# Optimization experiments

Hardware: AMD Instinct MI355X
Metric: run time of the kernel (lower is better)

## Reference

```python
import jax, jax.numpy as jnp
import numpy as np

N = 10000       # nodes
E = 640000      # edges (avg degree 64)
F_IN = 128      # num_node_features
H = 128         # hid_size
C = 16          # num_classes


def setup_inputs() -> dict:
    key = jax.random.key(0)
    ks = jax.random.split(key, 12)
    g = lambda k, shape, fan: jax.random.normal(k, shape, jnp.float32) * (1.0 / np.sqrt(fan))
    return {
        "x": jax.random.normal(ks[0], (N, F_IN), jnp.float32),
        "edge_index": jax.random.randint(ks[1], (2, E), 0, N, dtype=jnp.int32),
        "W1": g(ks[2], (F_IN, H), F_IN), "b1": jnp.zeros((H,), jnp.float32),
        "W2": g(ks[3], (H, H), H),       "b2": jnp.zeros((H,), jnp.float32),
        "Wlin1": g(ks[4], (H, C), H),    "blin1": jnp.zeros((C,), jnp.float32),
        "Wdeg2": g(ks[5], (H, 1), H),    "bdeg2": jnp.zeros((1,), jnp.float32),
        "Wdeg3": g(ks[6], (H, 1), H),    "bdeg3": jnp.zeros((1,), jnp.float32),
        "Wdown": g(ks[7], (F_IN, H), F_IN), "bdown": jnp.zeros((H,), jnp.float32),
    }


def _gcn_norm(edge_index):
    # PyG GCNConv: add self-loops, symmetric normalization d^-1/2 A d^-1/2
    loops = jnp.arange(N, dtype=edge_index.dtype)
    src = jnp.concatenate([edge_index[0], loops])   # [E+N]
    dst = jnp.concatenate([edge_index[1], loops])   # [E+N]
    deg = jax.ops.segment_sum(jnp.ones_like(dst, jnp.float32), dst, num_segments=N)
    dis = jnp.where(deg > 0, jax.lax.rsqrt(jnp.maximum(deg, 1.0)), 0.0)
    norm = dis[src] * dis[dst]                      # [E+N]
    return src, dst, norm


def _gcn_conv(h, W, b, src, dst, norm):
    h = h @ W                                       # [N, H] transform first (smaller dim)
    msg = h[src] * norm[:, None]                    # gather + edge weight
    return jax.ops.segment_sum(msg, dst, num_segments=N) + b


def reference(x, edge_index, W1, b1, W2, b2, Wlin1, blin1, Wdeg2, bdeg2, Wdeg3, bdeg3, Wdown, bdown):
    src, dst, norm = _gcn_norm(edge_index)
    original = x @ Wdown + bdown                    # down_sample residual
    h = jax.nn.relu(_gcn_conv(x, W1, b1, src, dst, norm))
    # dropout is identity in eval mode
    h = _gcn_conv(h, W2, b2, src, dst, norm) + original
    result1 = jax.nn.log_softmax(h @ Wlin1 + blin1, axis=1)   # [N, C]
    result2 = (h @ Wdeg2 + bdeg2)[:, 0]                        # [N]
    result3 = (h @ Wdeg3 + bdeg3)[:, 0]                        # [N]
    return (result1, result2, result3)
```

## Files before the change

kernel.cpp:

```cpp
#include <hip/hip_runtime.h>
#include <math.h>

#define N_NODES 10000
#define N_EDGES 640000
#define NB      100
#define CH      (N_EDGES / NB)
#define HP      10016
#define GB      313
#define NBLK    40
#define NPB2    250

typedef unsigned short ushort4_t __attribute__((ext_vector_type(4)));
typedef unsigned short ushort8_t __attribute__((ext_vector_type(8)));

__device__ inline unsigned short f2bf(float f) {
    unsigned int u = __float_as_uint(f);
    u = (u + 0x7FFFu + ((u >> 16) & 1u)) >> 16;
    return (unsigned short)u;
}
__device__ inline float bf2f(unsigned short s) {
    return __uint_as_float(((unsigned int)s) << 16);
}

__device__ __forceinline__ void gbar(int* bar, int slot, int nblk) {
    __syncthreads();
    if (threadIdx.x == 0) {
        int* cnt = bar + slot;
        int* gen = bar + 8 + slot;
        int g = atomicAdd(gen, 0);
        __threadfence();
        if (atomicAdd(cnt, 1) == nblk - 1) {
            __threadfence();
            atomicAdd(gen, 1);
        } else {
            while (atomicAdd(gen, 0) == g) __builtin_amdgcn_s_sleep(4);
        }
        __threadfence();
    }
    __syncthreads();
}

__global__ __launch_bounds__(256) void k_hist_gemm2(const int* __restrict__ dst,
                                                    unsigned short* __restrict__ hmat,
                                                    unsigned short* __restrict__ rank,
                                                    int* __restrict__ bar,
                                                    const float* __restrict__ X,
                                                    const float* __restrict__ W1,
                                                    const float* __restrict__ Wdown,
                                                    const float* __restrict__ bdown,
                                                    unsigned short* __restrict__ outT,
                                                    float* __restrict__ outB, int n) {
    __shared__ char smem[81920];
    int t = threadIdx.x;

    if (blockIdx.x < NB) {
        int* hs = (int*)smem;
        if (blockIdx.x == 0 && t < 16) bar[t] = 0;
        for (int j = t; j < HP; j += 256) hs[j] = 0;
        __syncthreads();
        int base = blockIdx.x * CH;
#pragma unroll 4
        for (int j = t; j < CH; j += 256) {
            int r = atomicAdd(&hs[dst[base + j]], 1);
            rank[base + j] = (unsigned short)r;
        }
        __syncthreads();
        unsigned short* out = hmat + blockIdx.x * HP;
        for (int j = t; j < N_NODES; j += 256) out[j] = (unsigned short)hs[j];
        return;
    }

    float* xs = (float*)smem;
    float* wsm = (float*)(smem + 16384);
    int bid = blockIdx.x - NB;
    int which = (bid >= GB) ? 1 : 0;
    int bx = which ? bid - GB : bid;
    int tile0 = bx * 32;
    const float* W = which ? Wdown : W1;

    const float4* Wv = (const float4*)W;
    float4* wsv = (float4*)wsm;
#pragma unroll
    for (int q = 0; q < 16; ++q) wsv[t + 256 * q] = Wv[t + 256 * q];

    const float4* Xv = (const float4*)X;
    float4* xsv = (float4*)xs;
#pragma unroll
    for (int q = 0; q < 4; ++q) {
        int idx = t + 256 * q;
        int row = tile0 + (idx >> 5);
        float4 v = make_float4(0.f, 0.f, 0.f, 0.f);
        if (row < n) v = Xv[(size_t)row * 32 + (idx & 31)];
        xsv[idx] = v;
    }
    __syncthreads();

    int c4 = t & 31;
    int rg = t >> 5;
    float4 acc[4];
#pragma unroll
    for (int p = 0; p < 4; ++p) acc[p] = make_float4(0.f, 0.f, 0.f, 0.f);

    const float4* wsr = (const float4*)wsm;
    const float4* xsr = (const float4*)xs;
#pragma unroll 4
    for (int kq = 0; kq < 32; ++kq) {
        float4 w0 = wsr[(4 * kq + 0) * 32 + c4];
        float4 w1 = wsr[(4 * kq + 1) * 32 + c4];
        float4 w2 = wsr[(4 * kq + 2) * 32 + c4];
        float4 w3 = wsr[(4 * kq + 3) * 32 + c4];
#pragma unroll
        for (int p = 0; p < 4; ++p) {
            float4 xv = xsr[(rg * 4 + p) * 32 + kq];
            acc[p].x += xv.x * w0.x + xv.y * w1.x + xv.z * w2.x + xv.w * w3.x;
            acc[p].y += xv.x * w0.y + xv.y * w1.y + xv.z * w2.y + xv.w * w3.y;
            acc[p].z += xv.x * w0.z + xv.y * w1.z + xv.z * w2.z + xv.w * w3.z;
            acc[p].w += xv.x * w0.w + xv.y * w1.w + xv.z * w2.w + xv.w * w3.w;
        }
    }
    if (which == 0) {
#pragma unroll
        for (int p = 0; p < 4; ++p) {
            int row = tile0 + rg * 4 + p;
            if (row < n) {
                ushort4_t o;
                o[0] = f2bf(acc[p].x); o[1] = f2bf(acc[p].y);
                o[2] = f2bf(acc[p].z); o[3] = f2bf(acc[p].w);
                ((ushort4_t*)outT)[(size_t)row * 32 + c4] = o;
            }
        }
    } else {
        float4 bv = ((const float4*)bdown)[c4];
#pragma unroll
        for (int p = 0; p < 4; ++p) {
            int row = tile0 + rg * 4 + p;
            if (row < n) {
                float4 o;
                o.x = acc[p].x + bv.x; o.y = acc[p].y + bv.y;
                o.z = acc[p].z + bv.z; o.w = acc[p].w + bv.w;
                ((float4*)outB)[(size_t)row * 32 + c4] = o;
            }
        }
    }
}

__global__ __launch_bounds__(256) void k_mid(const unsigned short* __restrict__ h,
                                             int* bar,
                                             int* __restrict__ rangesum,
                                             int* __restrict__ offsets,
                                             float* __restrict__ dis,
                                             int* __restrict__ bmat) {
    __shared__ int sc[256];
    __shared__ int rsl[NBLK];
    __shared__ int sP;
    int b = blockIdx.x, t = threadIdx.x;
    int i = b * NPB2 + t;
    bool act = (t < NPB2);

    int s = 0;
    if (act) {
#pragma unroll 10
        for (int bb = 0; bb < NB; ++bb) s += h[bb * HP + i];
        dis[i] = rsqrtf((float)(s + 1));
    }
    sc[t] = s;
    __syncthreads();
#pragma unroll
    for (int off = 1; off < 256; off <<= 1) {
        int v = (t >= off) ? sc[t - off] : 0;
        __syncthreads();
        sc[t] += v;
        __syncthreads();
    }
    int lofs = sc[t] - s;
    if (t == 255) rangesum[b] = sc[255];
    gbar(bar, 0, NBLK);

    if (t < NBLK) rsl[t] = rangesum[t];
    __syncthreads();
    if (t == 0) {
        int P = 0;
        for (int bb = 0; bb < b; ++bb) P += rsl[bb];
        sP = P;
        if (b == NBLK - 1) offsets[N_NODES] = P + rsl[b];
    }
    __syncthreads();
    if (act) {
        int run = sP + lofs;
        offsets[i] = run;
#pragma unroll 10
        for (int bb = 0; bb < NB; ++bb) {
            bmat[bb * HP + i] = run;
            run += h[bb * HP + i];
        }
    }
}

__global__ __launch_bounds__(256) void k_scatter_ep(const int* __restrict__ src,
                                                    const int* __restrict__ dst,
                                                    const unsigned short* __restrict__ rank,
                                                    const int* __restrict__ bmat,
                                                    const float* __restrict__ dis,
                                                    int2* __restrict__ rec) {
    int e = blockIdx.x * 256 + threadIdx.x;
    int b = blockIdx.x / (CH / 256);
    int d = dst[e];
    int s = src[e];
    int r = rank[e];
    int pos = bmat[b * HP + d] + r;
    rec[pos] = make_int2(s, __float_as_int(dis[s]));
}

__global__ __launch_bounds__(256) void k_gemm(const float* __restrict__ X,
                                              const float* __restrict__ W,
                                              unsigned short* __restrict__ Y, int n) {
    __shared__ float xs[32 * 128];
    __shared__ float ws[128 * 128];
    int t = threadIdx.x;
    int tile0 = blockIdx.x * 32;

    const float4* Wv = (const float4*)W;
    float4* wsv = (float4*)ws;
#pragma unroll
    for (int q = 0; q < 16; ++q) wsv[t + 256 * q] = Wv[t + 256 * q];

    const float4* Xv = (const float4*)X;
    float4* xsv = (float4*)xs;
#pragma unroll
    for (int q = 0; q < 4; ++q) {
        int idx = t + 256 * q;
        int row = tile0 + (idx >> 5);
        float4 v = make_float4(0.f, 0.f, 0.f, 0.f);
        if (row < n) v = Xv[(size_t)row * 32 + (idx & 31)];
        xsv[idx] = v;
    }
    __syncthreads();

    int c4 = t & 31;
    int rg = t >> 5;
    float4 acc[4];
#pragma unroll
    for (int p = 0; p < 4; ++p) acc[p] = make_float4(0.f, 0.f, 0.f, 0.f);

    const float4* wsr = (const float4*)ws;
    const float4* xsr = (const float4*)xs;
#pragma unroll 4
    for (int kq = 0; kq < 32; ++kq) {
        float4 w0 = wsr[(4 * kq + 0) * 32 + c4];
        float4 w1 = wsr[(4 * kq + 1) * 32 + c4];
        float4 w2 = wsr[(4 * kq + 2) * 32 + c4];
        float4 w3 = wsr[(4 * kq + 3) * 32 + c4];
#pragma unroll
        for (int p = 0; p < 4; ++p) {
            float4 xv = xsr[(rg * 4 + p) * 32 + kq];
            acc[p].x += xv.x * w0.x + xv.y * w1.x + xv.z * w2.x + xv.w * w3.x;
            acc[p].y += xv.x * w0.y + xv.y * w1.y + xv.z * w2.y + xv.w * w3.y;
            acc[p].z += xv.x * w0.z + xv.y * w1.z + xv.z * w2.z + xv.w * w3.z;
            acc[p].w += xv.x * w0.w + xv.y * w1.w + xv.z * w2.w + xv.w * w3.w;
        }
    }
#pragma unroll
    for (int p = 0; p < 4; ++p) {
        int row = tile0 + rg * 4 + p;
        if (row < n) {
            ushort4_t o;
            o[0] = f2bf(acc[p].x); o[1] = f2bf(acc[p].y);
            o[2] = f2bf(acc[p].z); o[3] = f2bf(acc[p].w);
            ((ushort4_t*)Y)[(size_t)row * 32 + c4] = o;
        }
    }
}

#define AGG_EDGE_LOOP_B                                                        \
    float acc[8];                                                              \
    _Pragma("unroll") for (int j = 0; j < 8; ++j) acc[j] = 0.f;                \
    int e = e0 + es;                                                           \
    for (; e + 48 < e1; e += 64) {                                             \
        int2 r0 = rec[e], r1 = rec[e + 16], r2 = rec[e + 32], r3 = rec[e + 48];\
        float w0 = __int_as_float(r0.y), w1 = __int_as_float(r1.y);            \
        float w2 = __int_as_float(r2.y), w3 = __int_as_float(r3.y);            \
        ushort8_t v0 = T8[(size_t)r0.x * 16 + c8];                             \
        ushort8_t v1 = T8[(size_t)r1.x * 16 + c8];                             \
        ushort8_t v2 = T8[(size_t)r2.x * 16 + c8];                             \
        ushort8_t v3 = T8[(size_t)r3.x * 16 + c8];                             \
        _Pragma("unroll") for (int j = 0; j < 8; ++j)                          \
            acc[j] += w0 * bf2f(v0[j]) + w1 * bf2f(v1[j]) +                    \
                      w2 * bf2f(v2[j]) + w3 * bf2f(v3[j]);                     \
    }                                                                          \
    for (; e + 16 < e1; e += 32) {                                             \
        int2 r0 = rec[e], r1 = rec[e + 16];                                    \
        float w0 = __int_as_float(r0.y), w1 = __int_as_float(r1.y);            \
        ushort8_t v0 = T8[(size_t)r0.x * 16 + c8];                             \
        ushort8_t v1 = T8[(size_t)r1.x * 16 + c8];                             \
        _Pragma("unroll") for (int j = 0; j < 8; ++j)                          \
            acc[j] += w0 * bf2f(v0[j]) + w1 * bf2f(v1[j]);                     \
    }                                                                          \
    if (e < e1) {                                                              \
        int2 r0 = rec[e];                                                      \
        float w0 = __int_as_float(r0.y);                                       \
        ushort8_t v0 = T8[(size_t)r0.x * 16 + c8];                             \
        _Pragma("unroll") for (int j = 0; j < 8; ++j)                          \
            acc[j] += w0 * bf2f(v0[j]);                                        \
    }                                                                          \
    _Pragma("unroll") for (int j = 0; j < 8; ++j) {                            \
        acc[j] += __shfl_xor(acc[j], 16, 64);                                  \
        acc[j] += __shfl_xor(acc[j], 32, 64);                                  \
    }

__global__ __launch_bounds__(256) void k_agg1(const ushort8_t* __restrict__ T8,
                                              const float* __restrict__ dis,
                                              const int* __restrict__ offsets,
                                              const int2* __restrict__ rec,
                                              const float* __restrict__ bias,
                                              float* __restrict__ Y) {
    __shared__ float red[3][16][9];
    int i = blockIdx.x;
    int t = threadIdx.x;
    int c8 = t & 15;
    int es = t >> 4;
    int wave = t >> 6;
    int lane = t & 63;
    int e0 = offsets[i], e1 = offsets[i + 1];

    AGG_EDGE_LOOP_B

    if (wave > 0 && lane < 16) {
#pragma unroll
        for (int j = 0; j < 8; ++j) red[wave - 1][lane][j] = acc[j];
    }
    __syncthreads();
    if (wave == 0 && lane < 16) {
#pragma unroll
        for (int j = 0; j < 8; ++j)
            acc[j] += red[0][lane][j] + red[1][lane][j] + red[2][lane][j];

        float di = dis[i];
        ushort8_t sv = T8[(size_t)i * 16 + c8];
#pragma unroll
        for (int j = 0; j < 8; ++j) acc[j] += di * bf2f(sv[j]);
#pragma unroll
        for (int j = 0; j < 8; ++j)
            acc[j] = fmaxf(di * acc[j] + bias[c8 * 8 + j], 0.f);

        float4* Y4 = (float4*)Y;
        Y4[(size_t)i * 32 + c8 * 2]     = make_float4(acc[0], acc[1], acc[2], acc[3]);
        Y4[(size_t)i * 32 + c8 * 2 + 1] = make_float4(acc[4], acc[5], acc[6], acc[7]);
    }
}

__global__ __launch_bounds__(256) void k_agg2h(const ushort8_t* __restrict__ T8,
                                               const float* __restrict__ dis,
                                               const int* __restrict__ offsets,
                                               const int2* __restrict__ rec,
                                               const float* __restrict__ bias,
                                               const float* __restrict__ resid,
                                               const float* __restrict__ Wlin,
                                               const float* __restrict__ blin,
                                               const float* __restrict__ Wd2,
                                               const float* __restrict__ bd2,
                                               const float* __restrict__ Wd3,
                                               const float* __restrict__ bd3,
                                               float* __restrict__ out1,
                                               float* __restrict__ out2,
                                               float* __restrict__ out3) {
    __shared__ float red[3][16][9];
    __shared__ float hrow[128];
    int i = blockIdx.x;
    int t = threadIdx.x;
    int c8 = t & 15;
    int es = t >> 4;
    int wave = t >> 6;
    int lane = t & 63;
    int e0 = offsets[i], e1 = offsets[i + 1];

    AGG_EDGE_LOOP_B

    if (wave > 0 && lane < 16) {
#pragma unroll
        for (int j = 0; j < 8; ++j) red[wave - 1][lane][j] = acc[j];
    }
    __syncthreads();
    if (wave == 0 && lane < 16) {
#pragma unroll
        for (int j = 0; j < 8; ++j)
            acc[j] += red[0][lane][j] + red[1][lane][j] + red[2][lane][j];

        float di = dis[i];
        ushort8_t sv = T8[(size_t)i * 16 + c8];
#pragma unroll
        for (int j = 0; j < 8; ++j) acc[j] += di * bf2f(sv[j]);

        const float4* rv4 = (const float4*)resid;
        float4 r0 = rv4[(size_t)i * 32 + c8 * 2];
        float4 r1 = rv4[(size_t)i * 32 + c8 * 2 + 1];
#pragma unroll
        for (int j = 0; j < 8; ++j) acc[j] = di * acc[j] + bias[c8 * 8 + j];
        acc[0] += r0.x; acc[1] += r0.y; acc[2] += r0.z; acc[3] += r0.w;
        acc[4] += r1.x; acc[5] += r1.y; acc[6] += r1.z; acc[7] += r1.w;

#pragma unroll
        for (int j = 0; j < 8; ++j) hrow[c8 * 8 + j] = acc[j];
    }
    __syncthreads();

    if (wave == 0) {
        float h0 = hrow[lane];
        float h1 = hrow[64 + lane];
        float p2 = h0 * Wd2[lane] + h1 * Wd2[64 + lane];
        float p3 = h0 * Wd3[lane] + h1 * Wd3[64 + lane];
#pragma unroll
        for (int d = 1; d < 64; d <<= 1) {
            p2 += __shfl_xor(p2, d, 64);
            p3 += __shfl_xor(p3, d, 64);
        }
        if (lane == 0) {
            out2[i] = p2 + bd2[0];
            out3[i] = p3 + bd3[0];
        }
        int c = lane & 15, kg = lane >> 4;
        float z = 0.f;
#pragma unroll 8
        for (int j = 0; j < 32; ++j) {
            int k = kg * 32 + j;
            z += hrow[k] * Wlin[k * 16 + c];
        }
        z += __shfl_xor(z, 16, 64);
        z += __shfl_xor(z, 32, 64);
        z += blin[c];
        float m = z;
#pragma unroll
        for (int d = 1; d < 16; d <<= 1) m = fmaxf(m, __shfl_xor(m, d, 64));
        float ex = expf(z - m);
        float ssum = ex;
#pragma unroll
        for (int d = 1; d < 16; d <<= 1) ssum += __shfl_xor(ssum, d, 64);
        float lsm = z - m - logf(ssum);
        if (lane < 16) out1[(size_t)i * 16 + c] = lsm;
    }
}

extern "C" void kernel_launch(void* const* d_in, const int* in_sizes, int n_in,
                              void* d_out, int out_size, void* d_ws, size_t ws_size,
                              hipStream_t stream) {
    const float* x     = (const float*)d_in[0];
    const int*   ei    = (const int*)d_in[1];
    const float* W1    = (const float*)d_in[2];
    const float* b1    = (const float*)d_in[3];
    const float* W2    = (const float*)d_in[4];
    const float* b2    = (const float*)d_in[5];
    const float* Wlin1 = (const float*)d_in[6];
    const float* blin1 = (const float*)d_in[7];
    const float* Wdeg2 = (const float*)d_in[8];
    const float* bdeg2 = (const float*)d_in[9];
    const float* Wdeg3 = (const float*)d_in[10];
    const float* bdeg3 = (const float*)d_in[11];
    const float* Wdown = (const float*)d_in[12];
    const float* bdown = (const float*)d_in[13];

    const int n = N_NODES, E = N_EDGES;
    const int* src = ei;
    const int* dst = ei + E;

    char* ws = (char*)d_ws;
    int*            bar      = (int*)ws;
    unsigned short* hmat     = (unsigned short*)(bar + 64);
    int*            bmat     = (int*)(hmat + NB * HP);
    int*            rangesum = bmat + NB * HP;
    int*            offsets  = rangesum + 64;
    float*          dis      = (float*)(offsets + 10048);
    unsigned short* rank     = (unsigned short*)(dis + HP);
    int2*           rec      = (int2*)(rank + E);
    unsigned short* bufT     = (unsigned short*)(rec + E);
    float*          bufB     = (float*)(bufT + (size_t)n * 128);
    float*          bufC     = bufB + (size_t)n * 128;

    k_hist_gemm2<<<NB + 2 * GB, 256, 0, stream>>>(dst, hmat, rank, bar, x, W1,
                                                  Wdown, bdown, bufT, bufB, n);
    k_mid<<<NBLK, 256, 0, stream>>>(hmat, bar, rangesum, offsets, dis, bmat);
    k_scatter_ep<<<E / 256, 256, 0, stream>>>(src, dst, rank, bmat, dis, rec);
    k_agg1<<<n, 256, 0, stream>>>((const ushort8_t*)bufT, dis, offsets, rec,
                                  b1, bufC);
    k_gemm<<<(n + 31) / 32, 256, 0, stream>>>(bufC, W2, bufT, n);
    float* out1 = (float*)d_out;
    float* out2 = out1 + (size_t)n * 16;
    float* out3 = out2 + n;
    k_agg2h<<<n, 256, 0, stream>>>((const ushort8_t*)bufT, dis, offsets, rec,
                                   b2, bufB, Wlin1, blin1, Wdeg2, bdeg2,
                                   Wdeg3, bdeg3, out1, out2, out3);
}
```

Baseline: 104.9 us.

## Fuse graph-build stages and agg1+GEMM into kernels joined by inter-block flags

```diff
diff --git a/kernel.cpp b/kernel.cpp
--- a/kernel.cpp
+++ b/kernel.cpp
@@ -9,6 +9,7 @@
 #define GB      313
 #define NBLK    40
 #define NPB2    250
+#define MID0    (NB + 2 * GB)
 
 typedef unsigned short ushort4_t __attribute__((ext_vector_type(4)));
 typedef unsigned short ushort8_t __attribute__((ext_vector_type(8)));
@@ -40,127 +41,139 @@
     __syncthreads();
 }
 
-__global__ __launch_bounds__(256) void k_hist_gemm2(const int* __restrict__ dst,
-                                                    unsigned short* __restrict__ hmat,
-                                                    unsigned short* __restrict__ rank,
-                                                    int* __restrict__ bar,
-                                                    const float* __restrict__ X,
-                                                    const float* __restrict__ W1,
-                                                    const float* __restrict__ Wdown,
-                                                    const float* __restrict__ bdown,
-                                                    unsigned short* __restrict__ outT,
-                                                    float* __restrict__ outB, int n) {
+__global__ __launch_bounds__(256) void k_front(const int* __restrict__ dst,
+                                               unsigned short* __restrict__ hmat,
+                                               unsigned short* __restrict__ rank,
+                                               int* bar,
+                                               const float* __restrict__ X,
+                                               const float* __restrict__ W1,
+                                               const float* __restrict__ Wdown,
+                                               const float* __restrict__ bdown,
+                                               unsigned short* __restrict__ outT,
+                                               float* __restrict__ outB,
+                                               int* __restrict__ rangesum,
+                                               int* __restrict__ offsets,
+                                               float* __restrict__ dis,
+                                               int* __restrict__ bmat, int n) {
     __shared__ char smem[81920];
     int t = threadIdx.x;
-
-    if (blockIdx.x < NB) {
+    int bid = blockIdx.x;
+
+    if (bid < NB) {
         int* hs = (int*)smem;
-        if (blockIdx.x == 0 && t < 16) bar[t] = 0;
+        if (bid == 0 && t < 16) bar[t] = 0;
         for (int j = t; j < HP; j += 256) hs[j] = 0;
         __syncthreads();
-        int base = blockIdx.x * CH;
+        int base = bid * CH;
 #pragma unroll 4
         for (int j = t; j < CH; j += 256) {
             int r = atomicAdd(&hs[dst[base + j]], 1);
             rank[base + j] = (unsigned short)r;
         }
         __syncthreads();
-        unsigned short* out = hmat + blockIdx.x * HP;
+        unsigned short* out = hmat + bid * HP;
         for (int j = t; j < N_NODES; j += 256) out[j] = (unsigned short)hs[j];
+        __syncthreads();
+        if (t == 0) {
+            __threadfence();
+            atomicExch(&bar[16 + bid], 1);
+        }
         return;
     }
 
-    float* xs = (float*)smem;
-    float* wsm = (float*)(smem + 16384);
-    int bid = blockIdx.x - NB;
-    int which = (bid >= GB) ? 1 : 0;
-    int bx = which ? bid - GB : bid;
-    int tile0 = bx * 32;
-    const float* W = which ? Wdown : W1;
-
-    const float4* Wv = (const float4*)W;
-    float4* wsv = (float4*)wsm;
-#pragma unroll
-    for (int q = 0; q < 16; ++q) wsv[t + 256 * q] = Wv[t + 256 * q];
-
-    const float4* Xv = (const float4*)X;
-    float4* xsv = (float4*)xs;
-#pragma unroll
-    for (int q = 0; q < 4; ++q) {
-        int idx = t + 256 * q;
-        int row = tile0 + (idx >> 5);
-        float4 v = make_float4(0.f, 0.f, 0.f, 0.f);
-        if (row < n) v = Xv[(size_t)row * 32 + (idx & 31)];
-        xsv[idx] = v;
-    }
-    __syncthreads();
-
-    int c4 = t & 31;
-    int rg = t >> 5;
-    float4 acc[4];
-#pragma unroll
-    for (int p = 0; p < 4; ++p) acc[p] = make_float4(0.f, 0.f, 0.f, 0.f);
-
-    const float4* wsr = (const float4*)wsm;
-    const float4* xsr = (const float4*)xs;
+    if (bid < MID0) {
+        float* xs = (float*)smem;
+        float* wsm = (float*)(smem + 16384);
+        int gid = bid - NB;
+        int which = (gid >= GB) ? 1 : 0;
+        int bx = which ? gid - GB : gid;
+        int tile0 = bx * 32;
+        const float* W = which ? Wdown : W1;
+
+        const float4* Wv = (const float4*)W;
+        float4* wsv = (float4*)wsm;
+#pragma unroll
+        for (int q = 0; q < 16; ++q) wsv[t + 256 * q] = Wv[t + 256 * q];
+
+        const float4* Xv = (const float4*)X;
+        float4* xsv = (float4*)xs;
+#pragma unroll
+        for (int q = 0; q < 4; ++q) {
+            int idx = t + 256 * q;
+            int row = tile0 + (idx >> 5);
+            float4 v = make_float4(0.f, 0.f, 0.f, 0.f);
+            if (row < n) v = Xv[(size_t)row * 32 + (idx & 31)];
+            xsv[idx] = v;
+        }
+        __syncthreads();
+
+        int c4 = t & 31;
+        int rg = t >> 5;
+        float4 acc[4];
+#pragma unroll
+        for (int p = 0; p < 4; ++p) acc[p] = make_float4(0.f, 0.f, 0.f, 0.f);
+
+        const float4* wsr = (const float4*)wsm;
+        const float4* xsr = (const float4*)xs;
 #pragma unroll 4
-    for (int kq = 0; kq < 32; ++kq) {
-        float4 w0 = wsr[(4 * kq + 0) * 32 + c4];
-        float4 w1 = wsr[(4 * kq + 1) * 32 + c4];
-        float4 w2 = wsr[(4 * kq + 2) * 32 + c4];
-        float4 w3 = wsr[(4 * kq + 3) * 32 + c4];
-#pragma unroll
-        for (int p = 0; p < 4; ++p) {
-            float4 xv = xsr[(rg * 4 + p) * 32 + kq];
-            acc[p].x += xv.x * w0.x + xv.y * w1.x + xv.z * w2.x + xv.w * w3.x;
-            acc[p].y += xv.x * w0.y + xv.y * w1.y + xv.z * w2.y + xv.w * w3.y;
-            acc[p].z += xv.x * w0.z + xv.y * w1.z + xv.z * w2.z + xv.w * w3.z;
-            acc[p].w += xv.x * w0.w + xv.y * w1.w + xv.z * w2.w + xv.w * w3.w;
-        }
-    }
-    if (which == 0) {
-#pragma unroll
-        for (int p = 0; p < 4; ++p) {
-            int row = tile0 + rg * 4 + p;
-            if (row < n) {
-                ushort4_t o;
-                o[0] = f2bf(acc[p].x); o[1] = f2bf(acc[p].y);
-                o[2] = f2bf(acc[p].z); o[3] = f2bf(acc[p].w);
-                ((ushort4_t*)outT)[(size_t)row * 32 + c4] = o;
+        for (int kq = 0; kq < 32; ++kq) {
+            float4 w0 = wsr[(4 * kq + 0) * 32 + c4];
+            float4 w1 = wsr[(4 * kq + 1) * 32 + c4];
+            float4 w2 = wsr[(4 * kq + 2) * 32 + c4];
+            float4 w3 = wsr[(4 * kq + 3) * 32 + c4];
+#pragma unroll
+            for (int p = 0; p < 4; ++p) {
+                float4 xv = xsr[(rg * 4 + p) * 32 + kq];
+                acc[p].x += xv.x * w0.x + xv.y * w1.x + xv.z * w2.x + xv.w * w3.x;
+                acc[p].y += xv.x * w0.y + xv.y * w1.y + xv.z * w2.y + xv.w * w3.y;
+                acc[p].z += xv.x * w0.z + xv.y * w1.z + xv.z * w2.z + xv.w * w3.z;
+                acc[p].w += xv.x * w0.w + xv.y * w1.w + xv.z * w2.w + xv.w * w3.w;
             }
         }
-    } else {
-        float4 bv = ((const float4*)bdown)[c4];
-#pragma unroll
-        for (int p = 0; p < 4; ++p) {
-            int row = tile0 + rg * 4 + p;
-            if (row < n) {
-                float4 o;
-                o.x = acc[p].x + bv.x; o.y = acc[p].y + bv.y;
-                o.z = acc[p].z + bv.z; o.w = acc[p].w + bv.w;
-                ((float4*)outB)[(size_t)row * 32 + c4] = o;
+        if (which == 0) {
+#pragma unroll
+            for (int p = 0; p < 4; ++p) {
+                int row = tile0 + rg * 4 + p;
+                if (row < n) {
+                    ushort4_t o;
+                    o[0] = f2bf(acc[p].x); o[1] = f2bf(acc[p].y);
+                    o[2] = f2bf(acc[p].z); o[3] = f2bf(acc[p].w);
+                    ((ushort4_t*)outT)[(size_t)row * 32 + c4] = o;
+                }
             }
-        }
-    }
-}
-
-__global__ __launch_bounds__(256) void k_mid(const unsigned short* __restrict__ h,
-                                             int* bar,
-                                             int* __restrict__ rangesum,
-                                             int* __restrict__ offsets,
-                                             float* __restrict__ dis,
-                                             int* __restrict__ bmat) {
-    __shared__ int sc[256];
-    __shared__ int rsl[NBLK];
-    __shared__ int sP;
-    int b = blockIdx.x, t = threadIdx.x;
-    int i = b * NPB2 + t;
+        } else {
+            float4 bv = ((const float4*)bdown)[c4];
+#pragma unroll
+            for (int p = 0; p < 4; ++p) {
+                int row = tile0 + rg * 4 + p;
+                if (row < n) {
+                    float4 o;
+                    o.x = acc[p].x + bv.x; o.y = acc[p].y + bv.y;
+                    o.z = acc[p].z + bv.z; o.w = acc[p].w + bv.w;
+                    ((float4*)outB)[(size_t)row * 32 + c4] = o;
+                }
+            }
+        }
+        return;
+    }
+
+    int mb = bid - MID0;
+    if (t < NB) {
+        while (atomicAdd(&bar[16 + t], 0) != 1) __builtin_amdgcn_s_sleep(8);
+    }
+    __syncthreads();
+    __threadfence();
+
+    int* sc  = (int*)smem;
+    int* rsl = (int*)smem + 256;
+    int* sPp = (int*)smem + 256 + 64;
+    int i = mb * NPB2 + t;
     bool act = (t < NPB2);
 
     int s = 0;
     if (act) {
 #pragma unroll 10
-        for (int bb = 0; bb < NB; ++bb) s += h[bb * HP + i];
+        for (int bb = 0; bb < NB; ++bb) s += hmat[bb * HP + i];
         dis[i] = rsqrtf((float)(s + 1));
     }
     sc[t] = s;
@@ -173,25 +186,25 @@
         __syncthreads();
     }
     int lofs = sc[t] - s;
-    if (t == 255) rangesum[b] = sc[255];
+    if (t == 255) rangesum[mb] = sc[255];
     gbar(bar, 0, NBLK);
 
     if (t < NBLK) rsl[t] = rangesum[t];
     __syncthreads();
     if (t == 0) {
         int P = 0;
-        for (int bb = 0; bb < b; ++bb) P += rsl[bb];
-        sP = P;
-        if (b == NBLK - 1) offsets[N_NODES] = P + rsl[b];
+        for (int bb = 0; bb < mb; ++bb) P += rsl[bb];
+        sPp[0] = P;
+        if (mb == NBLK - 1) offsets[N_NODES] = P + rsl[mb];
     }
     __syncthreads();
     if (act) {
-        int run = sP + lofs;
+        int run = sPp[0] + lofs;
         offsets[i] = run;
 #pragma unroll 10
         for (int bb = 0; bb < NB; ++bb) {
             bmat[bb * HP + i] = run;
-            run += h[bb * HP + i];
+            run += hmat[bb * HP + i];
         }
     }
 }
@@ -201,7 +214,10 @@
                                                     const unsigned short* __restrict__ rank,
                                                     const int* __restrict__ bmat,
                                                     const float* __restrict__ dis,
-                                                    int2* __restrict__ rec) {
+                                                    int2* __restrict__ rec,
+                                                    int* bar) {
+    if (blockIdx.x == 0 && threadIdx.x < NB + 1)
+        atomicExch(&bar[16 + threadIdx.x], 0);
     int e = blockIdx.x * 256 + threadIdx.x;
     int b = blockIdx.x / (CH / 256);
     int d = dst[e];
@@ -209,66 +225,6 @@
     int r = rank[e];
     int pos = bmat[b * HP + d] + r;
     rec[pos] = make_int2(s, __float_as_int(dis[s]));
-}
-
-__global__ __launch_bounds__(256) void k_gemm(const float* __restrict__ X,
-                                              const float* __restrict__ W,
-                                              unsigned short* __restrict__ Y, int n) {
-    __shared__ float xs[32 * 128];
-    __shared__ float ws[128 * 128];
-    int t = threadIdx.x;
-    int tile0 = blockIdx.x * 32;
-
-    const float4* Wv = (const float4*)W;
-    float4* wsv = (float4*)ws;
-#pragma unroll
-    for (int q = 0; q < 16; ++q) wsv[t + 256 * q] = Wv[t + 256 * q];
-
-    const float4* Xv = (const float4*)X;
-    float4* xsv = (float4*)xs;
-#pragma unroll
-    for (int q = 0; q < 4; ++q) {
-        int idx = t + 256 * q;
-        int row = tile0 + (idx >> 5);
-        float4 v = make_float4(0.f, 0.f, 0.f, 0.f);
-        if (row < n) v = Xv[(size_t)row * 32 + (idx & 31)];
-        xsv[idx] = v;
-    }
-    __syncthreads();
-
-    int c4 = t & 31;
-    int rg = t >> 5;
-    float4 acc[4];
-#pragma unroll
-    for (int p = 0; p < 4; ++p) acc[p] = make_float4(0.f, 0.f, 0.f, 0.f);
-
-    const float4* wsr = (const float4*)ws;
-    const float4* xsr = (const float4*)xs;
-#pragma unroll 4
-    for (int kq = 0; kq < 32; ++kq) {
-        float4 w0 = wsr[(4 * kq + 0) * 32 + c4];
-        float4 w1 = wsr[(4 * kq + 1) * 32 + c4];
-        float4 w2 = wsr[(4 * kq + 2) * 32 + c4];
-        float4 w3 = wsr[(4 * kq + 3) * 32 + c4];
-#pragma unroll
-        for (int p = 0; p < 4; ++p) {
-            float4 xv = xsr[(rg * 4 + p) * 32 + kq];
-            acc[p].x += xv.x * w0.x + xv.y * w1.x + xv.z * w2.x + xv.w * w3.x;
-            acc[p].y += xv.x * w0.y + xv.y * w1.y + xv.z * w2.y + xv.w * w3.y;
-            acc[p].z += xv.x * w0.z + xv.y * w1.z + xv.z * w2.z + xv.w * w3.z;
-            acc[p].w += xv.x * w0.w + xv.y * w1.w + xv.z * w2.w + xv.w * w3.w;
-        }
-    }
-#pragma unroll
-    for (int p = 0; p < 4; ++p) {
-        int row = tile0 + rg * 4 + p;
-        if (row < n) {
-            ushort4_t o;
-            o[0] = f2bf(acc[p].x); o[1] = f2bf(acc[p].y);
-            o[2] = f2bf(acc[p].z); o[3] = f2bf(acc[p].w);
-            ((ushort4_t*)Y)[(size_t)row * 32 + c4] = o;
-        }
-    }
 }
 
 #define AGG_EDGE_LOOP_B                                                        \
@@ -307,44 +263,113 @@
         acc[j] += __shfl_xor(acc[j], 32, 64);                                  \
     }
 
-__global__ __launch_bounds__(256) void k_agg1(const ushort8_t* __restrict__ T8,
-                                              const float* __restrict__ dis,
-                                              const int* __restrict__ offsets,
-                                              const int2* __restrict__ rec,
-                                              const float* __restrict__ bias,
-                                              float* __restrict__ Y) {
-    __shared__ float red[3][16][9];
-    int i = blockIdx.x;
+__global__ __launch_bounds__(256) void k_agg1_gemm(const ushort8_t* __restrict__ T8,
+                                                   const float* __restrict__ dis,
+                                                   const int* __restrict__ offsets,
+                                                   const int2* __restrict__ rec,
+                                                   const float* __restrict__ bias,
+                                                   const float* __restrict__ W2,
+                                                   float* __restrict__ h1out,
+                                                   unsigned short* __restrict__ outT2,
+                                                   int* bar, int n) {
+    __shared__ char smem[16384];
+    int bid = blockIdx.x;
     int t = threadIdx.x;
-    int c8 = t & 15;
-    int es = t >> 4;
-    int wave = t >> 6;
-    int lane = t & 63;
-    int e0 = offsets[i], e1 = offsets[i + 1];
-
-    AGG_EDGE_LOOP_B
-
-    if (wave > 0 && lane < 16) {
-#pragma unroll
-        for (int j = 0; j < 8; ++j) red[wave - 1][lane][j] = acc[j];
-    }
-    __syncthreads();
-    if (wave == 0 && lane < 16) {
-#pragma unroll
-        for (int j = 0; j < 8; ++j)
-            acc[j] += red[0][lane][j] + red[1][lane][j] + red[2][lane][j];
-
-        float di = dis[i];
-        ushort8_t sv = T8[(size_t)i * 16 + c8];
-#pragma unroll
-        for (int j = 0; j < 8; ++j) acc[j] += di * bf2f(sv[j]);
-#pragma unroll
-        for (int j = 0; j < 8; ++j)
-            acc[j] = fmaxf(di * acc[j] + bias[c8 * 8 + j], 0.f);
-
-        float4* Y4 = (float4*)Y;
-        Y4[(size_t)i * 32 + c8 * 2]     = make_float4(acc[0], acc[1], acc[2], acc[3]);
-        Y4[(size_t)i * 32 + c8 * 2 + 1] = make_float4(acc[4], acc[5], acc[6], acc[7]);
+
+    if (bid < n) {
+        float (*red)[16][9] = (float (*)[16][9])smem;
+        int i = bid;
+        int c8 = t & 15;
+        int es = t >> 4;
+        int wave = t >> 6;
+        int lane = t & 63;
+        int e0 = offsets[i], e1 = offsets[i + 1];
+
+        AGG_EDGE_LOOP_B
+
+        if (wave > 0 && lane < 16) {
+#pragma unroll
+            for (int j = 0; j < 8; ++j) red[wave - 1][lane][j] = acc[j];
+        }
+        __syncthreads();
+        if (wave == 0 && lane < 16) {
+#pragma unroll
+            for (int j = 0; j < 8; ++j)
+                acc[j] += red[0][lane][j] + red[1][lane][j] + red[2][lane][j];
+
+            float di = dis[i];
+            ushort8_t sv = T8[(size_t)i * 16 + c8];
+#pragma unroll
+            for (int j = 0; j < 8; ++j) acc[j] += di * bf2f(sv[j]);
+#pragma unroll
+            for (int j = 0; j < 8; ++j)
+                acc[j] = fmaxf(di * acc[j] + bias[c8 * 8 + j], 0.f);
+
+            float4* Y4 = (float4*)h1out;
+            Y4[(size_t)i * 32 + c8 * 2]     = make_float4(acc[0], acc[1], acc[2], acc[3]);
+            Y4[(size_t)i * 32 + c8 * 2 + 1] = make_float4(acc[4], acc[5], acc[6], acc[7]);
+        }
+        __syncthreads();
+        if (t == 0) {
+            __threadfence();
+            atomicAdd(&bar[116], 1);
+        }
+        return;
+    }
+
+    if (t == 0) {
+        while (atomicAdd(&bar[116], 0) < n) __builtin_amdgcn_s_sleep(8);
+    }
+    __syncthreads();
+    __threadfence();
+
+    float* xs = (float*)smem;
+    int tile0 = (bid - n) * 32;
+
+    const float4* Xv = (const float4*)h1out;
+    float4* xsv = (float4*)xs;
+#pragma unroll
+    for (int q = 0; q < 4; ++q) {
+        int idx = t + 256 * q;
+        int row = tile0 + (idx >> 5);
+        float4 v = make_float4(0.f, 0.f, 0.f, 0.f);
+        if (row < n) v = Xv[(size_t)row * 32 + (idx & 31)];
+        xsv[idx] = v;
+    }
+    __syncthreads();
+
+    int c4 = t & 31;
+    int rg = t >> 5;
+    float4 acc[4];
+#pragma unroll
+    for (int p = 0; p < 4; ++p) acc[p] = make_float4(0.f, 0.f, 0.f, 0.f);
+
+    const float4* Wv = (const float4*)W2;
+    const float4* xsr = (const float4*)xs;
+#pragma unroll 4
+    for (int kq = 0; kq < 32; ++kq) {
+        float4 w0 = Wv[(4 * kq + 0) * 32 + c4];
+        float4 w1 = Wv[(4 * kq + 1) * 32 + c4];
+        float4 w2 = Wv[(4 * kq + 2) * 32 + c4];
+        float4 w3 = Wv[(4 * kq + 3) * 32 + c4];
+#pragma unroll
+        for (int p = 0; p < 4; ++p) {
+            float4 xv = xsr[(rg * 4 + p) * 32 + kq];
+            acc[p].x += xv.x * w0.x + xv.y * w1.x + xv.z * w2.x + xv.w * w3.x;
+            acc[p].y += xv.x * w0.y + xv.y * w1.y + xv.z * w2.y + xv.w * w3.y;
+            acc[p].z += xv.x * w0.z + xv.y * w1.z + xv.z * w2.z + xv.w * w3.z;
+            acc[p].w += xv.x * w0.w + xv.y * w1.w + xv.z * w2.w + xv.w * w3.w;
+        }
+    }
+#pragma unroll
+    for (int p = 0; p < 4; ++p) {
+        int row = tile0 + rg * 4 + p;
+        if (row < n) {
+            ushort4_t o;
+            o[0] = f2bf(acc[p].x); o[1] = f2bf(acc[p].y);
+            o[2] = f2bf(acc[p].z); o[3] = f2bf(acc[p].w);
+            ((ushort4_t*)outT2)[(size_t)row * 32 + c4] = o;
+        }
     }
 }
 
@@ -463,7 +488,7 @@
 
     char* ws = (char*)d_ws;
     int*            bar      = (int*)ws;
-    unsigned short* hmat     = (unsigned short*)(bar + 64);
+    unsigned short* hmat     = (unsigned short*)(bar + 128);
     int*            bmat     = (int*)(hmat + NB * HP);
     int*            rangesum = bmat + NB * HP;
     int*            offsets  = rangesum + 64;
@@ -474,13 +499,12 @@
     float*          bufB     = (float*)(bufT + (size_t)n * 128);
     float*          bufC     = bufB + (size_t)n * 128;
 
-    k_hist_gemm2<<<NB + 2 * GB, 256, 0, stream>>>(dst, hmat, rank, bar, x, W1,
-                                                  Wdown, bdown, bufT, bufB, n);
-    k_mid<<<NBLK, 256, 0, stream>>>(hmat, bar, rangesum, offsets, dis, bmat);
-    k_scatter_ep<<<E / 256, 256, 0, stream>>>(src, dst, rank, bmat, dis, rec);
-    k_agg1<<<n, 256, 0, stream>>>((const ushort8_t*)bufT, dis, offsets, rec,
-                                  b1, bufC);
-    k_gemm<<<(n + 31) / 32, 256, 0, stream>>>(bufC, W2, bufT, n);
+    k_front<<<MID0 + NBLK, 256, 0, stream>>>(dst, hmat, rank, bar, x, W1, Wdown,
+                                             bdown, bufT, bufB, rangesum,
+                                             offsets, dis, bmat, n);
+    k_scatter_ep<<<E / 256, 256, 0, stream>>>(src, dst, rank, bmat, dis, rec, bar);
+    k_agg1_gemm<<<n + GB, 256, 0, stream>>>((const ushort8_t*)bufT, dis, offsets,
+                                            rec, b1, W2, bufC, bufT, bar, n);
     float* out1 = (float*)d_out;
     float* out2 = out1 + (size_t)n * 16;
     float* out3 = out2 + n;
```

Result: slower. 409.0 us (+289.8%).
